# Optimization experiments

Hardware: AMD Instinct MI355X
Metric: run time of the kernel (lower is better)

Reference implementation:

```python
import jax, jax.numpy as jnp
import numpy as np

T, O, H, A = 8192, 1024, 2048, 512


def setup_inputs() -> dict:
    key = jax.random.key(0)
    ks = jax.random.split(key, 9)
    sc = 1.0 / np.sqrt(H)
    g = lambda k, shape: (jax.random.normal(k, shape, dtype=jnp.float32) * sc)
    return {
        "obs": jax.random.normal(ks[0], (T, O), dtype=jnp.float32),
        "W_ih": g(ks[1], (3 * H, O)),
        "W_hh": g(ks[2], (3 * H, H)),
        "b_ih": g(ks[3], (3 * H,)),
        "b_hh": g(ks[4], (3 * H,)),
        "W_o": g(ks[5], (A, H)),
        "b_o": g(ks[6], (A,)),
        "W_d": g(ks[7], (A, H)),
        "b_d": g(ks[8], (A,)),
    }


def _gru_hidden_states(obs, W_ih, W_hh, b_ih, b_hh):
    """Run a PyTorch-style GRUCell over obs (T, O); return all hidden states (T, H)."""
    h_dim = W_hh.shape[1]
    # Input projections for all timesteps at once (one big GEMM instead of T GEMVs).
    gx = obs @ W_ih.T + b_ih  # (T, 3H), gate order r, z, n

    def step(h, gx_t):
        gh = h @ W_hh.T + b_hh  # (3H,)
        r = jax.nn.sigmoid(gx_t[:h_dim] + gh[:h_dim])
        z = jax.nn.sigmoid(gx_t[h_dim:2 * h_dim] + gh[h_dim:2 * h_dim])
        n = jnp.tanh(gx_t[2 * h_dim:] + r * gh[2 * h_dim:])
        h_new = (1.0 - z) * n + z * h
        return h_new, h_new

    h0 = jnp.zeros((h_dim,), dtype=obs.dtype)
    _, hs = jax.lax.scan(step, h0, gx)
    return hs  # hs[t] == h_{t+1} in the torch code


def reference(obs, W_ih, W_hh, b_ih, b_hh, W_o, b_o, W_d, b_d):
    hs = _gru_hidden_states(obs, W_ih, W_hh, b_ih, b_hh)  # (T, H)
    h_last = hs[-1]          # (H,)  == h[-1].T column
    h_mid = hs[:-1]          # (T-1, H) == cat(h[1:-1])
    attention = jax.nn.softmax(h_mid @ h_last, axis=0)  # (T-1,)
    c = jnp.sum(h_mid * attention[:, None], axis=0)      # (H,)
    o_logits = c @ W_o.T + b_o  # (A,)
    d_logits = c @ W_d.T + b_d  # (A,)
    return (o_logits, d_logits)
```

## Files before the change

### kernel.cpp

```cpp
#include <hip/hip_runtime.h>
#include <hip/hip_bf16.h>

#define T_DIM 8192
#define O_DIM 1024
#define H_DIM 2048
#define G_DIM 6144
#define A_DIM 512
#define CHUNK 512
#define NBLK 256

#define OFF_GXC   0ull
#define OFF_HTAG  3145728ull
#define OFF_S     3153920ull
#define OFF_RED   3162112ull
#define OFF_CPART 3162128ull
#define OFF_C     3293200ull
#define OFF_HSBF  3295248ull

__device__ __forceinline__ float bf2f(unsigned short u) {
  return __uint_as_float(((unsigned)u) << 16);
}
__device__ __forceinline__ unsigned packbf(float a, float b) {
  return (unsigned)__bfloat16_as_ushort(__float2bfloat16(a)) |
         ((unsigned)__bfloat16_as_ushort(__float2bfloat16(b)) << 16);
}

#define BM 64
#define BN 64
#define BK 16
__global__ __launch_bounds__(256) void gemm_gx(
    const float* __restrict__ A,
    const float* __restrict__ B,
    const float* __restrict__ bias,
    float* __restrict__ C) {
  __shared__ float As[BM][BK + 1];
  __shared__ float Bs[BN][BK + 1];
  const int bm = blockIdx.x * BM;
  const int bn = blockIdx.y * BN;
  const int tid = threadIdx.x;
  const int tr = tid / 16, tc = tid % 16;
  float acc[4][4] = {};
  for (int k0 = 0; k0 < O_DIM; k0 += BK) {
    for (int i = tid; i < BM * BK; i += 256) {
      int r = i / BK, c = i % BK;
      As[r][c] = A[(size_t)(bm + r) * O_DIM + k0 + c];
    }
    for (int i = tid; i < BN * BK; i += 256) {
      int r = i / BK, c = i % BK;
      Bs[r][c] = B[(size_t)(bn + r) * O_DIM + k0 + c];
    }
    __syncthreads();
#pragma unroll
    for (int kk = 0; kk < BK; ++kk) {
      float a[4], b[4];
#pragma unroll
      for (int i = 0; i < 4; ++i) a[i] = As[tr * 4 + i][kk];
#pragma unroll
      for (int j = 0; j < 4; ++j) b[j] = Bs[tc * 4 + j][kk];
#pragma unroll
      for (int i = 0; i < 4; ++i)
#pragma unroll
        for (int j = 0; j < 4; ++j) acc[i][j] += a[i] * b[j];
    }
    __syncthreads();
  }
#pragma unroll
  for (int i = 0; i < 4; ++i)
#pragma unroll
    for (int j = 0; j < 4; ++j) {
      int r = bm + tr * 4 + i, cc = bn + tc * 4 + j;
      C[(size_t)r * G_DIM + cc] = acc[i][j] + bias[cc];
    }
}

#define DOTQ(Q, ACC)                                                  \
  do {                                                                \
    ACC += __uint_as_float((Q).x << 16)          * ha.x               \
         + __uint_as_float((Q).x & 0xffff0000u)  * ha.y               \
         + __uint_as_float((Q).y << 16)          * ha.z               \
         + __uint_as_float((Q).y & 0xffff0000u)  * ha.w               \
         + __uint_as_float((Q).z << 16)          * hb.x               \
         + __uint_as_float((Q).z & 0xffff0000u)  * hb.y               \
         + __uint_as_float((Q).w << 16)          * hb.z               \
         + __uint_as_float((Q).w & 0xffff0000u)  * hb.w;              \
  } while (0)

__global__ __launch_bounds__(512, 2) void scan_chunk(
    const float* __restrict__ W_hh,
    const float* __restrict__ b_hh,
    const float* __restrict__ gxc,
    unsigned long long* __restrict__ htag,
    unsigned short* __restrict__ hsbf16,
    int t0, int nsteps) {
  __shared__ char smem[98304];
  float* hlbuf0 = (float*)smem;
  float* hlbuf1 = (float*)(smem + 8192);
  unsigned long long* stage = (unsigned long long*)(smem + 16384);
  const int tid = threadIdx.x;
  const int lane = tid & 63;
  const int wv = tid >> 6;
  const int blk = blockIdx.x;
  const int u = blk * 8 + wv;

  const float4* wr0 = (const float4*)(W_hh + (size_t)(0 * H_DIM + u) * H_DIM);
  const float4* wr1 = (const float4*)(W_hh + (size_t)(1 * H_DIM + u) * H_DIM);
  const float4* wr2 = (const float4*)(W_hh + (size_t)(2 * H_DIM + u) * H_DIM);
#define LOADQ(WR, J2)                                                  \
  ({ const float4 lo = (WR)[lane + 128 * (J2)];                        \
     const float4 hi = (WR)[lane + 64 + 128 * (J2)];                   \
     uint4{packbf(lo.x, lo.y), packbf(lo.z, lo.w),                     \
           packbf(hi.x, hi.y), packbf(hi.z, hi.w)}; })
  const uint4 q00 = LOADQ(wr0, 0), q01 = LOADQ(wr0, 1),
              q02 = LOADQ(wr0, 2), q03 = LOADQ(wr0, 3);
  const uint4 q10 = LOADQ(wr1, 0), q11 = LOADQ(wr1, 1),
              q12 = LOADQ(wr1, 2), q13 = LOADQ(wr1, 3);
  const uint4 q20 = LOADQ(wr2, 0), q21 = LOADQ(wr2, 1),
              q22 = LOADQ(wr2, 2), q23 = LOADQ(wr2, 3);
#undef LOADQ

  float b0 = 0.f, b1 = 0.f, b2 = 0.f;
  if (lane == 0) {
    b0 = b_hh[u]; b1 = b_hh[H_DIM + u]; b2 = b_hh[2 * H_DIM + u];
  }

  for (int tt = 0; tt < nsteps; ++tt) {
    const int t = t0 + tt;
    const unsigned long long* hin = htag + (size_t)(t & 1) * H_DIM;
    unsigned long long* hout = htag + (size_t)((t + 1) & 1) * H_DIM;
    float* hl = (t & 1) ? hlbuf1 : hlbuf0;

    float gx0 = 0.f, gx1 = 0.f, gx2 = 0.f;
    if (lane == 0) {
      const float* g = gxc + (size_t)tt * G_DIM + u;
      gx0 = g[0]; gx1 = g[H_DIM]; gx2 = g[2 * H_DIM];
    }

    unsigned long long v[4];
    const unsigned tgt = (unsigned)t;
    for (;;) {
      bool ok = true;
#pragma unroll
      for (int j = 0; j < 4; ++j) {
        v[j] = __hip_atomic_load(hin + tid + 512 * j,
                                 __ATOMIC_RELAXED, __HIP_MEMORY_SCOPE_AGENT);
        ok = ok && ((unsigned)v[j] >= tgt);
      }
      if (ok) break;
      __builtin_amdgcn_s_sleep(1);
    }
#pragma unroll
    for (int j = 0; j < 4; ++j)
      hl[tid + 512 * j] = __uint_as_float((unsigned)(v[j] >> 32));
    __syncthreads();

    float a0 = 0.f, a1 = 0.f, a2 = 0.f;
    const float4* h4 = (const float4*)hl;
    {
      float4 ha, hb;
      ha = h4[lane +   0]; hb = h4[lane +  64];
      DOTQ(q00, a0); DOTQ(q10, a1); DOTQ(q20, a2);
      ha = h4[lane + 128]; hb = h4[lane + 192];
      DOTQ(q01, a0); DOTQ(q11, a1); DOTQ(q21, a2);
      ha = h4[lane + 256]; hb = h4[lane + 320];
      DOTQ(q02, a0); DOTQ(q12, a1); DOTQ(q22, a2);
      ha = h4[lane + 384]; hb = h4[lane + 448];
      DOTQ(q03, a0); DOTQ(q13, a1); DOTQ(q23, a2);
    }
#pragma unroll
    for (int d = 32; d > 0; d >>= 1) {
      a0 += __shfl_xor(a0, d, 64);
      a1 += __shfl_xor(a1, d, 64);
      a2 += __shfl_xor(a2, d, 64);
    }

    float hnew = 0.f;
    if (lane == 0) {
      const float rr = 1.f / (1.f + expf(-(gx0 + a0 + b0)));
      const float zz = 1.f / (1.f + expf(-(gx1 + a1 + b1)));
      const float nn = tanhf(gx2 + rr * (a2 + b2));
      hnew = (1.f - zz) * nn + zz * hl[u];
      stage[wv] = ((unsigned long long)__float_as_uint(hnew) << 32) |
                  (unsigned long long)(unsigned)(t + 1);
    }
    __syncthreads();

    if (tid < 8) {
      __hip_atomic_store(hout + blk * 8 + tid, stage[tid],
                         __ATOMIC_RELAXED, __HIP_MEMORY_SCOPE_AGENT);
    }
    if (lane == 0) {
      hsbf16[(size_t)t * H_DIM + u] =
          (unsigned short)__bfloat16_as_ushort(__float2bfloat16(hnew));
    }
  }
}

__global__ __launch_bounds__(256) void attn_scores(
    const unsigned short* __restrict__ hs_bf,
    const unsigned long long* __restrict__ hq,
    float* __restrict__ s, int n) {
  __shared__ float hl[H_DIM];
  const int tid = threadIdx.x;
  for (int i = tid; i < H_DIM; i += 256)
    hl[i] = __uint_as_float((unsigned)(hq[i] >> 32));
  __syncthreads();
  const int wave = tid >> 6, lane = tid & 63;
  const int t = blockIdx.x * 4 + wave;
  if (t >= n) return;
  const uint4* r4 = (const uint4*)(hs_bf + (size_t)t * H_DIM);
  float sum = 0.f;
#pragma unroll
  for (int u = 0; u < 4; ++u) {
    const int idx = lane + 64 * u;
    uint4 v = r4[idx];
    const float* l = hl + idx * 8;
    sum += bf2f((unsigned short)(v.x & 0xffff)) * l[0];
    sum += bf2f((unsigned short)(v.x >> 16))    * l[1];
    sum += bf2f((unsigned short)(v.y & 0xffff)) * l[2];
    sum += bf2f((unsigned short)(v.y >> 16))    * l[3];
    sum += bf2f((unsigned short)(v.z & 0xffff)) * l[4];
    sum += bf2f((unsigned short)(v.z >> 16))    * l[5];
    sum += bf2f((unsigned short)(v.w & 0xffff)) * l[6];
    sum += bf2f((unsigned short)(v.w >> 16))    * l[7];
  }
#pragma unroll
  for (int d = 32; d > 0; d >>= 1) sum += __shfl_xor(sum, d, 64);
  if (lane == 0) s[t] = sum;
}

__global__ __launch_bounds__(1024) void softmax_stats(
    const float* __restrict__ s, int n, float* __restrict__ red) {
  __shared__ float buf[1024];
  const int tid = threadIdx.x;
  float m = -3.4e38f;
  for (int i = tid; i < n; i += 1024) m = fmaxf(m, s[i]);
  buf[tid] = m;
  __syncthreads();
  for (int d = 512; d > 0; d >>= 1) {
    if (tid < d) buf[tid] = fmaxf(buf[tid], buf[tid + d]);
    __syncthreads();
  }
  const float mm = buf[0];
  __syncthreads();
  float sum = 0.f;
  for (int i = tid; i < n; i += 1024) sum += expf(s[i] - mm);
  buf[tid] = sum;
  __syncthreads();
  for (int d = 512; d > 0; d >>= 1) {
    if (tid < d) buf[tid] += buf[tid + d];
    __syncthreads();
  }
  if (tid == 0) { red[0] = mm; red[1] = buf[0]; }
}

__global__ __launch_bounds__(256) void attn_wsum(
    const unsigned short* __restrict__ hs_bf, const float* __restrict__ s,
    const float* __restrict__ red, float* __restrict__ c_part, int n) {
  const int tid = threadIdx.x;
  const float m = red[0];
  const float inv = 1.f / red[1];
  const int tchunk = (n + 63) / 64;
  const int t0 = blockIdx.x * tchunk;
  const int t1 = min(t0 + tchunk, n);
  float acc[8] = {};
  for (int t = t0; t < t1; ++t) {
    const float w = expf(s[t] - m) * inv;
    const uint4 v = ((const uint4*)(hs_bf + (size_t)t * H_DIM))[tid];
    acc[0] += w * bf2f((unsigned short)(v.x & 0xffff));
    acc[1] += w * bf2f((unsigned short)(v.x >> 16));
    acc[2] += w * bf2f((unsigned short)(v.y & 0xffff));
    acc[3] += w * bf2f((unsigned short)(v.y >> 16));
    acc[4] += w * bf2f((unsigned short)(v.z & 0xffff));
    acc[5] += w * bf2f((unsigned short)(v.z >> 16));
    acc[6] += w * bf2f((unsigned short)(v.w & 0xffff));
    acc[7] += w * bf2f((unsigned short)(v.w >> 16));
  }
  float* dst = c_part + (size_t)blockIdx.x * H_DIM + tid * 8;
#pragma unroll
  for (int k = 0; k < 8; ++k) dst[k] = acc[k];
}

__global__ __launch_bounds__(256) void reduce_c(
    const float* __restrict__ c_part, float* __restrict__ c) {
  const int i = blockIdx.x * 256 + threadIdx.x;
  float sum = 0.f;
  for (int b = 0; b < 64; ++b) sum += c_part[(size_t)b * H_DIM + i];
  c[i] = sum;
}

__global__ __launch_bounds__(64) void logits_kernel(
    const float* __restrict__ W_o, const float* __restrict__ b_o,
    const float* __restrict__ W_d, const float* __restrict__ b_d,
    const float* __restrict__ c, float* __restrict__ out) {
  const int j = blockIdx.x;
  const int lane = threadIdx.x;
  const float* W; const float* bb; int jj;
  if (j < A_DIM) { W = W_o; bb = b_o; jj = j; }
  else { W = W_d; bb = b_d; jj = j - A_DIM; }
  const float4* w4 = (const float4*)(W + (size_t)jj * H_DIM);
  const float4* c4 = (const float4*)c;
  float sum = 0.f;
#pragma unroll
  for (int u = 0; u < 8; ++u) {
    float4 a = w4[lane + 64 * u];
    float4 b = c4[lane + 64 * u];
    sum += a.x * b.x + a.y * b.y + a.z * b.z + a.w * b.w;
  }
#pragma unroll
  for (int d = 32; d > 0; d >>= 1) sum += __shfl_xor(sum, d, 64);
  if (lane == 0) out[j] = sum + bb[jj];
}

extern "C" void kernel_launch(void* const* d_in, const int* in_sizes, int n_in,
                              void* d_out, int out_size, void* d_ws, size_t ws_size,
                              hipStream_t stream) {
  const float* obs  = (const float*)d_in[0];
  const float* W_ih = (const float*)d_in[1];
  const float* W_hh = (const float*)d_in[2];
  const float* b_ih = (const float*)d_in[3];
  const float* b_hh = (const float*)d_in[4];
  const float* W_o  = (const float*)d_in[5];
  const float* b_o  = (const float*)d_in[6];
  const float* W_d  = (const float*)d_in[7];
  const float* b_d  = (const float*)d_in[8];
  float* out = (float*)d_out;
  float* ws = (float*)d_ws;

  float* gxc      = ws + OFF_GXC;
  unsigned long long* htag = (unsigned long long*)(ws + OFF_HTAG);
  float* s        = ws + OFF_S;
  float* red      = ws + OFF_RED;
  float* c_part   = ws + OFF_CPART;
  float* c        = ws + OFF_C;
  unsigned short* hsbf16 = (unsigned short*)(ws + OFF_HSBF);

  hipMemsetAsync(htag, 0, 2 * H_DIM * sizeof(unsigned long long), stream);

  for (int ci = 0; ci < T_DIM / CHUNK; ++ci) {
    gemm_gx<<<dim3(CHUNK / BM, G_DIM / BN), 256, 0, stream>>>(
        obs + (size_t)ci * CHUNK * O_DIM, W_ih, b_ih, gxc);
    scan_chunk<<<NBLK, 512, 0, stream>>>(
        W_hh, b_hh, gxc, htag, hsbf16, ci * CHUNK, CHUNK);
  }
  const unsigned long long* h_last = htag;

  const int n = T_DIM - 1;
  attn_scores<<<(n + 3) / 4, 256, 0, stream>>>(hsbf16, h_last, s, n);
  softmax_stats<<<1, 1024, 0, stream>>>(s, n, red);
  attn_wsum<<<64, 256, 0, stream>>>(hsbf16, s, red, c_part, n);
  reduce_c<<<H_DIM / 256, 256, 0, stream>>>(c_part, c);
  logits_kernel<<<2 * A_DIM, 64, 0, stream>>>(W_o, b_o, W_d, b_d, c, out);
}
```

Before: 23.01 ms.

## Pack hidden-state exchange as bf16 pairs and overlap the second-half wait with compute

The per-step global exchange of the hidden state now packs two bf16 values per tagged 64-bit word instead of one fp32 value. This halves the number of atomic polling loads each thread issues per timestep. The wait is split into two halves so the first half of the matvec starts before the second half of h has arrived. Each unit keeps its own fp32 hidden value in a register, and the final state goes to a separate fp32 buffer for the attention stage. The cost is that the recurrent matvec now consumes bf16-rounded h, which may add drift over the long recurrence, plus an extra block barrier per step.

```diff
diff --git a/kernel.cpp b/kernel.cpp
--- a/kernel.cpp
+++ b/kernel.cpp
@@ -11,11 +11,12 @@
 
 #define OFF_GXC   0ull
 #define OFF_HTAG  3145728ull
-#define OFF_S     3153920ull
-#define OFF_RED   3162112ull
-#define OFF_CPART 3162128ull
-#define OFF_C     3293200ull
-#define OFF_HSBF  3295248ull
+#define OFF_HFP   3153920ull
+#define OFF_S     3155968ull
+#define OFF_RED   3164160ull
+#define OFF_CPART 3164176ull
+#define OFF_C     3295248ull
+#define OFF_HSBF  3297296ull
 
 __device__ __forceinline__ float bf2f(unsigned short u) {
   return __uint_as_float(((unsigned)u) << 16);
@@ -90,12 +91,13 @@
     const float* __restrict__ b_hh,
     const float* __restrict__ gxc,
     unsigned long long* __restrict__ htag,
+    float* __restrict__ hfp,
     unsigned short* __restrict__ hsbf16,
     int t0, int nsteps) {
   __shared__ char smem[98304];
   float* hlbuf0 = (float*)smem;
   float* hlbuf1 = (float*)(smem + 8192);
-  unsigned long long* stage = (unsigned long long*)(smem + 16384);
+  unsigned* stage32 = (unsigned*)(smem + 16384);
   const int tid = threadIdx.x;
   const int lane = tid & 63;
   const int wv = tid >> 6;
@@ -118,15 +120,20 @@
               q22 = LOADQ(wr2, 2), q23 = LOADQ(wr2, 3);
 #undef LOADQ
 
-  float b0 = 0.f, b1 = 0.f, b2 = 0.f;
+  float b0 = 0.f, b1 = 0.f, b2 = 0.f, hreg = 0.f;
   if (lane == 0) {
     b0 = b_hh[u]; b1 = b_hh[H_DIM + u]; b2 = b_hh[2 * H_DIM + u];
-  }
+    hreg = hfp[u];
+  }
+
+  const int w0 = tid, w1 = tid + 512;
+  const int s0 = ((w0 >> 2) << 3) | (w0 & 3);
+  const int s1 = ((w1 >> 2) << 3) | (w1 & 3);
 
   for (int tt = 0; tt < nsteps; ++tt) {
     const int t = t0 + tt;
-    const unsigned long long* hin = htag + (size_t)(t & 1) * H_DIM;
-    unsigned long long* hout = htag + (size_t)((t + 1) & 1) * H_DIM;
+    const unsigned long long* hin = htag + (size_t)(t & 1) * 2048;
+    unsigned long long* hout = htag + (size_t)((t + 1) & 1) * 2048;
     float* hl = (t & 1) ? hlbuf1 : hlbuf0;
 
     float gx0 = 0.f, gx1 = 0.f, gx2 = 0.f;
@@ -135,22 +142,25 @@
       gx0 = g[0]; gx1 = g[H_DIM]; gx2 = g[2 * H_DIM];
     }
 
-    unsigned long long v[4];
     const unsigned tgt = (unsigned)t;
+    unsigned long long v0, v1 = 0;
+    bool ok1 = false;
     for (;;) {
-      bool ok = true;
-#pragma unroll
-      for (int j = 0; j < 4; ++j) {
-        v[j] = __hip_atomic_load(hin + tid + 512 * j,
-                                 __ATOMIC_RELAXED, __HIP_MEMORY_SCOPE_AGENT);
-        ok = ok && ((unsigned)v[j] >= tgt);
+      v0 = __hip_atomic_load(hin + s0, __ATOMIC_RELAXED, __HIP_MEMORY_SCOPE_AGENT);
+      if (!ok1) {
+        v1 = __hip_atomic_load(hin + s1, __ATOMIC_RELAXED, __HIP_MEMORY_SCOPE_AGENT);
+        ok1 = ((unsigned)v1 >= tgt);
       }
-      if (ok) break;
+      if ((unsigned)v0 >= tgt) break;
       __builtin_amdgcn_s_sleep(1);
     }
-#pragma unroll
-    for (int j = 0; j < 4; ++j)
-      hl[tid + 512 * j] = __uint_as_float((unsigned)(v[j] >> 32));
+    {
+      const unsigned hi = (unsigned)(v0 >> 32);
+      float2 st;
+      st.x = bf2f((unsigned short)(hi & 0xffff));
+      st.y = bf2f((unsigned short)(hi >> 16));
+      ((float2*)hl)[tid] = st;
+    }
     __syncthreads();
 
     float a0 = 0.f, a1 = 0.f, a2 = 0.f;
@@ -161,6 +171,24 @@
       DOTQ(q00, a0); DOTQ(q10, a1); DOTQ(q20, a2);
       ha = h4[lane + 128]; hb = h4[lane + 192];
       DOTQ(q01, a0); DOTQ(q11, a1); DOTQ(q21, a2);
+    }
+
+    while (!ok1) {
+      v1 = __hip_atomic_load(hin + s1, __ATOMIC_RELAXED, __HIP_MEMORY_SCOPE_AGENT);
+      ok1 = ((unsigned)v1 >= tgt);
+      if (!ok1) __builtin_amdgcn_s_sleep(1);
+    }
+    {
+      const unsigned hi = (unsigned)(v1 >> 32);
+      float2 st;
+      st.x = bf2f((unsigned short)(hi & 0xffff));
+      st.y = bf2f((unsigned short)(hi >> 16));
+      ((float2*)hl)[512 + tid] = st;
+    }
+    __syncthreads();
+
+    {
+      float4 ha, hb;
       ha = h4[lane + 256]; hb = h4[lane + 320];
       DOTQ(q02, a0); DOTQ(q12, a1); DOTQ(q22, a2);
       ha = h4[lane + 384]; hb = h4[lane + 448];
@@ -178,31 +206,35 @@
       const float rr = 1.f / (1.f + expf(-(gx0 + a0 + b0)));
       const float zz = 1.f / (1.f + expf(-(gx1 + a1 + b1)));
       const float nn = tanhf(gx2 + rr * (a2 + b2));
-      hnew = (1.f - zz) * nn + zz * hl[u];
-      stage[wv] = ((unsigned long long)__float_as_uint(hnew) << 32) |
-                  (unsigned long long)(unsigned)(t + 1);
+      hnew = (1.f - zz) * nn + zz * hreg;
+      hreg = hnew;
+      stage32[wv] = (unsigned)__bfloat16_as_ushort(__float2bfloat16(hnew));
     }
     __syncthreads();
 
     if (tid < 8) {
-      __hip_atomic_store(hout + blk * 8 + tid, stage[tid],
+      const int k = tid & 3;
+      const unsigned hi = stage32[2 * k] | (stage32[2 * k + 1] << 16);
+      const unsigned long long word =
+          ((unsigned long long)hi << 32) | (unsigned long long)(unsigned)(t + 1);
+      __hip_atomic_store(hout + blk * 8 + tid, word,
                          __ATOMIC_RELAXED, __HIP_MEMORY_SCOPE_AGENT);
     }
     if (lane == 0) {
       hsbf16[(size_t)t * H_DIM + u] =
           (unsigned short)__bfloat16_as_ushort(__float2bfloat16(hnew));
+      if (tt == nsteps - 1) hfp[u] = hnew;
     }
   }
 }
 
 __global__ __launch_bounds__(256) void attn_scores(
     const unsigned short* __restrict__ hs_bf,
-    const unsigned long long* __restrict__ hq,
+    const float* __restrict__ h_last,
     float* __restrict__ s, int n) {
   __shared__ float hl[H_DIM];
   const int tid = threadIdx.x;
-  for (int i = tid; i < H_DIM; i += 256)
-    hl[i] = __uint_as_float((unsigned)(hq[i] >> 32));
+  for (int i = tid; i < H_DIM; i += 256) hl[i] = h_last[i];
   __syncthreads();
   const int wave = tid >> 6, lane = tid & 63;
   const int t = blockIdx.x * 4 + wave;
@@ -328,24 +360,25 @@
 
   float* gxc      = ws + OFF_GXC;
   unsigned long long* htag = (unsigned long long*)(ws + OFF_HTAG);
+  float* hfp      = ws + OFF_HFP;
   float* s        = ws + OFF_S;
   float* red      = ws + OFF_RED;
   float* c_part   = ws + OFF_CPART;
   float* c        = ws + OFF_C;
   unsigned short* hsbf16 = (unsigned short*)(ws + OFF_HSBF);
 
-  hipMemsetAsync(htag, 0, 2 * H_DIM * sizeof(unsigned long long), stream);
+  hipMemsetAsync(htag, 0, 2 * 2048 * sizeof(unsigned long long), stream);
+  hipMemsetAsync(hfp, 0, H_DIM * sizeof(float), stream);
 
   for (int ci = 0; ci < T_DIM / CHUNK; ++ci) {
     gemm_gx<<<dim3(CHUNK / BM, G_DIM / BN), 256, 0, stream>>>(
         obs + (size_t)ci * CHUNK * O_DIM, W_ih, b_ih, gxc);
     scan_chunk<<<NBLK, 512, 0, stream>>>(
-        W_hh, b_hh, gxc, htag, hsbf16, ci * CHUNK, CHUNK);
-  }
-  const unsigned long long* h_last = htag;
+        W_hh, b_hh, gxc, htag, hfp, hsbf16, ci * CHUNK, CHUNK);
+  }
 
   const int n = T_DIM - 1;
-  attn_scores<<<(n + 3) / 4, 256, 0, stream>>>(hsbf16, h_last, s, n);
+  attn_scores<<<(n + 3) / 4, 256, 0, stream>>>(hsbf16, hfp, s, n);
   softmax_stats<<<1, 1024, 0, stream>>>(s, n, red);
   attn_wsum<<<64, 256, 0, stream>>>(hsbf16, s, red, c_part, n);
   reduce_c<<<H_DIM / 256, 256, 0, stream>>>(c_part, c);
```

Measured after the change: 23.92 ms. 1.04x slower.
